# Optimization experiments

Hardware: AMD Instinct MI355X
Metric: run time of the kernel (lower is better)

Reference implementation:

```python
import jax, jax.numpy as jnp
import numpy as np

TAU = 0.8
LAMBDA_BALANCE = 0.05
EPS = 1e-8


def setup_inputs() -> dict:
    key = jax.random.key(0)
    ks = jax.random.split(key, 8)
    B, Din, Dh, Dout, E = 8192, 1024, 2048, 1024, 8
    x = jax.random.normal(ks[0], (B, Din), jnp.float32)
    # gumbel noise for F.gumbel_softmax: g = -log(-log(U)), U~Uniform(0,1)
    u = jax.random.uniform(ks[1], (B, E), jnp.float32, 1e-6, 1.0 - 1e-6)
    gumbel = -jnp.log(-jnp.log(u))
    gate_w = jax.random.normal(ks[2], (Din, E), jnp.float32) * 0.02
    gate_b = jnp.zeros((E,), jnp.float32)
    w1 = jax.random.normal(ks[3], (E, Din, Dh), jnp.float32) * (1.0 / np.sqrt(Din))
    b1 = jnp.zeros((E, Dh), jnp.float32)
    w2 = jax.random.normal(ks[4], (E, Dh, Dout), jnp.float32) * (1.0 / np.sqrt(Dh))
    b2 = jnp.zeros((E, Dout), jnp.float32)
    return dict(x=x, gumbel=gumbel, gate_w=gate_w, gate_b=gate_b,
                w1=w1, b1=b1, w2=w2, b2=b2)


def reference(x, gumbel, gate_w, gate_b, w1, b1, w2, b2):
    # gating logits [B, E]
    logits = x @ gate_w + gate_b
    # gumbel-softmax (soft), tau=0.8 -> selection probs (selection_policy='soft')
    probs = jax.nn.softmax((logits + gumbel) / TAU, axis=1)
    # load-balancing auxiliary loss
    router_probs = jax.nn.softmax(logits / TAU, axis=1)
    importance = router_probs.mean(axis=0)  # [E]
    load = probs.mean(axis=0)               # [E]
    importance_cv = jnp.std(importance, ddof=1) / (importance.mean() + EPS)
    load_cv = jnp.std(load, ddof=1) / (load.mean() + EPS)
    E = probs.shape[1]
    switch_loss = E * jnp.sum(importance * load)
    aux_loss = (switch_loss + importance_cv + load_cv) * LAMBDA_BALANCE
    # dense all-expert MLP stack: h [E,B,Dh], eo [E,B,Dout]
    h = jax.nn.relu(jnp.einsum('bd,edh->ebh', x, w1) + b1[:, None, :])
    eo = jnp.einsum('ebh,eho->ebo', h, w2) + b2[:, None, :]
    # bmm combine: expert_outputs [B, Dout, E] @ probs [B, E, 1] -> [B, Dout]
    output = jnp.einsum('ebo,be->bo', eo, probs)
    return output, aux_loss
```

## Files before the change

### kernel.cpp

```cpp
#include <hip/hip_runtime.h>

typedef __attribute__((ext_vector_type(4))) float f4;
typedef __attribute__((ext_vector_type(8))) short s8;

__device__ inline float b2f(unsigned int u) {
    unsigned int v = u << 16;
    float f;
    __builtin_memcpy(&f, &v, 4);
    return f;
}
__device__ inline unsigned short f2b(float f) {
    unsigned int u;
    __builtin_memcpy(&u, &f, 4);
    unsigned int r = u + 0x7fffu + ((u >> 16) & 1u);
    return (unsigned short)(r >> 16);
}
__device__ inline void async16(const void* g, void* l) {
    __builtin_amdgcn_global_load_lds(
        (const __attribute__((address_space(1))) unsigned int*)g,
        (__attribute__((address_space(3))) unsigned int*)l, 16, 0, 0);
}

#define B_ROWS 8192
#define DIN 1024
#define DH 2048
#define DOUT 1024
#define NE 8
#define NCAT 16384

#define MFMA16(a, b, c) __builtin_amdgcn_mfma_f32_16x16x32_bf16(a, b, c, 0, 0, 0)

__global__ __launch_bounds__(64) void detect_dtype(const unsigned short* __restrict__ p, int* __restrict__ flag)
{
    const int lane = threadIdx.x;
    int sane = 0;
    for (int i = lane; i < 4096; i += 64) {
        const float a = fabsf(b2f(p[i]));
        if (a > 1e-30f && a < 1e3f) sane++;
    }
    for (int off = 32; off; off >>= 1) sane += __shfl_xor(sane, off, 64);
    if (lane == 0) *flag = (sane < 3600) ? 1 : 0;
}

__global__ __launch_bounds__(256) void normalize_kernel(const void* __restrict__ src,
                                                        unsigned short* __restrict__ dst,
                                                        const int* __restrict__ flag, int n)
{
    const int i = blockIdx.x * 256 + threadIdx.x;
    if (i >= n) return;
    if (*flag) dst[i] = f2b(((const float*)src)[i]);
    else       dst[i] = ((const unsigned short*)src)[i];
}

__global__ __launch_bounds__(256) void gating_kernel(
    const unsigned short* __restrict__ x, const unsigned short* __restrict__ gum,
    const unsigned short* __restrict__ gw, const unsigned short* __restrict__ gb,
    float* __restrict__ probs, float* __restrict__ partials)
{
    const int t = threadIdx.x, wave = t >> 6, lane = t & 63;
    float sp = 0.f, sr = 0.f;
    const int base = blockIdx.x * 32 + wave * 8;
    for (int rr = 0; rr < 8; rr++) {
        const int b = base + rr;
        float acc[8];
#pragma unroll
        for (int e = 0; e < 8; e++) acc[e] = 0.f;
        for (int kk = 0; kk < 16; kk++) {
            const int k = kk * 64 + lane;
            const float xv = b2f(x[(size_t)b * DIN + k]);
            const uint4 wv = *(const uint4*)(gw + (size_t)k * 8);
            acc[0] += xv * b2f(wv.x & 0xffffu); acc[1] += xv * b2f(wv.x >> 16);
            acc[2] += xv * b2f(wv.y & 0xffffu); acc[3] += xv * b2f(wv.y >> 16);
            acc[4] += xv * b2f(wv.z & 0xffffu); acc[5] += xv * b2f(wv.z >> 16);
            acc[6] += xv * b2f(wv.w & 0xffffu); acc[7] += xv * b2f(wv.w >> 16);
        }
#pragma unroll
        for (int e = 0; e < 8; e++)
            for (int off = 32; off; off >>= 1) acc[e] += __shfl_xor(acc[e], off, 64);
        float lg[8], p1[8], p2[8];
        float m1 = -1e30f, m2 = -1e30f;
#pragma unroll
        for (int e = 0; e < 8; e++) {
            lg[e] = acc[e] + b2f(gb[e]);
            p1[e] = (lg[e] + b2f(gum[(size_t)b * 8 + e])) * 1.25f;
            p2[e] = lg[e] * 1.25f;
            m1 = fmaxf(m1, p1[e]); m2 = fmaxf(m2, p2[e]);
        }
        float s1 = 0.f, s2 = 0.f;
#pragma unroll
        for (int e = 0; e < 8; e++) {
            p1[e] = expf(p1[e] - m1); s1 += p1[e];
            p2[e] = expf(p2[e] - m2); s2 += p2[e];
        }
        const float i1 = 1.f / s1, i2 = 1.f / s2;
        if (lane < 8) {
            const float pv = p1[lane] * i1;
            probs[(size_t)b * 8 + lane] = pv;
            sp += pv;
            sr += p2[lane] * i2;
        }
    }
    __shared__ float red[4][16];
    if (lane < 8) { red[wave][lane] = sp; red[wave][8 + lane] = sr; }
    __syncthreads();
    if (t < 16)
        partials[blockIdx.x * 16 + t] = red[0][t] + red[1][t] + red[2][t] + red[3][t];
}

__global__ void aux_finalize(const float* __restrict__ partials, void* __restrict__ outp,
                             const int* __restrict__ flag)
{
    __shared__ float fin[16];
    const int t = threadIdx.x;
    if (t < 16) {
        float s = 0.f;
        for (int i = 0; i < 256; i++) s += partials[i * 16 + t];
        fin[t] = s;
    }
    __syncthreads();
    if (t == 0) {
        float ld[8], im[8];
        for (int e = 0; e < 8; e++) { ld[e] = fin[e] / 8192.f; im[e] = fin[8 + e] / 8192.f; }
        float mi = 0.f, ml = 0.f;
        for (int e = 0; e < 8; e++) { mi += im[e]; ml += ld[e]; }
        mi *= 0.125f; ml *= 0.125f;
        float vi = 0.f, vl = 0.f, sw = 0.f;
        for (int e = 0; e < 8; e++) {
            vi += (im[e] - mi) * (im[e] - mi);
            vl += (ld[e] - ml) * (ld[e] - ml);
            sw += im[e] * ld[e];
        }
        const float cvi = sqrtf(vi / 7.f) / (mi + 1e-8f);
        const float cvl = sqrtf(vl / 7.f) / (ml + 1e-8f);
        const float aux = (8.f * sw + cvi + cvl) * 0.05f;
        if (*flag) ((float*)outp)[8388608] = aux;
        else       ((unsigned short*)outp)[8388608] = f2b(aux);
    }
}

__global__ __launch_bounds__(256) void transpose_cvt(
    const void* __restrict__ src, unsigned short* __restrict__ out,
    int R, int C, int ldOut, size_t outEStride, const int* __restrict__ flag)
{
    __shared__ unsigned short tile[64][65];
    const int e = blockIdx.z;
    const size_t eoff = (size_t)e * R * C;
    unsigned short* op = out + (size_t)e * outEStride;
    const int fl = *flag;
    const int tx = threadIdx.x, ty = threadIdx.y;
    const int r0 = blockIdx.y * 64, c0 = blockIdx.x * 64;
    if (fl) {
        const float* in = (const float*)src + eoff;
#pragma unroll
        for (int i = 0; i < 16; i++) {
            const int r = ty + i * 4;
            tile[r][tx] = f2b(in[(size_t)(r0 + r) * C + c0 + tx]);
        }
    } else {
        const unsigned short* in = (const unsigned short*)src + eoff;
#pragma unroll
        for (int i = 0; i < 16; i++) {
            const int r = ty + i * 4;
            tile[r][tx] = in[(size_t)(r0 + r) * C + c0 + tx];
        }
    }
    __syncthreads();
#pragma unroll
    for (int i = 0; i < 16; i++) {
        const int c = ty + i * 4;
        op[(size_t)(c0 + c) * ldOut + r0 + tx] = tile[tx][c];
    }
}


__global__ __launch_bounds__(256) void gemm_h(
    const unsigned short* __restrict__ A,
    const unsigned short* __restrict__ Bt,
    const unsigned short* __restrict__ bias,
    const float* __restrict__ probs,
    unsigned short* __restrict__ outH)
{
    constexpr int K = DIN;
    __shared__ __align__(16) char smem[32768];

    const int t = threadIdx.x;
    int bid = blockIdx.y * gridDim.x + blockIdx.x;
    const int cpx = (gridDim.x * gridDim.y) >> 3;
    bid = (bid & 7) * cpx + (bid >> 3);
    const int bx = bid % gridDim.x, by = bid / gridDim.x;
    const int m0 = bx * 128, n0 = by * 128;

    const int wave = t >> 6, lane = t & 63;
    const int wm = wave >> 1, wn = wave & 1;
    const int quad = lane >> 4, l16 = lane & 15;

    f4 acc[4][4];
#pragma unroll
    for (int i = 0; i < 4; i++)
#pragma unroll
        for (int j = 0; j < 4; j++) { acc[i][j][0] = 0.f; acc[i][j][1] = 0.f; acc[i][j][2] = 0.f; acc[i][j][3] = 0.f; }

    const int rA = t >> 2;
    const int cb = (((t & 3) ^ ((t >> 3) & 3)) * 16);
    const char* pA0 = (const char*)(A + (size_t)(m0 + rA) * K) + cb;
    const char* pA1 = pA0 + (size_t)64 * K * 2;
    const char* pB0 = (const char*)(Bt + (size_t)(n0 + rA) * K) + cb;
    const char* pB1 = pB0 + (size_t)64 * K * 2;

    const int skey = ((quad ^ ((l16 >> 1) & 3)) << 4);
    int aoff[4], boff[4];
#pragma unroll
    for (int i = 0; i < 4; i++) {
        aoff[i] = (wm * 64 + i * 16 + l16) * 64 + skey;
        boff[i] = (wn * 64 + i * 16 + l16) * 64 + skey;
    }

    {
        char* s = smem;
        async16(pA0, s + t * 16);
        async16(pA1, s + 4096 + t * 16);
        async16(pB0, s + 8192 + t * 16);
        async16(pB1, s + 12288 + t * 16);
    }
    __syncthreads();

    int cur = 0;
    for (int k0 = 0; k0 < K; k0 += 32) {
        if (k0 + 32 < K) {
            char* s = smem + (cur ^ 1) * 16384;
            const size_t kb = (size_t)(k0 + 32) * 2;
            async16(pA0 + kb, s + t * 16);
            async16(pA1 + kb, s + 4096 + t * 16);
            async16(pB0 + kb, s + 8192 + t * 16);
            async16(pB1 + kb, s + 12288 + t * 16);
        }
        const char* s = smem + cur * 16384;
        s8 av[4], bv[4];
#pragma unroll
        for (int i = 0; i < 4; i++) av[i] = *(const s8*)(s + aoff[i]);
#pragma unroll
        for (int j = 0; j < 4; j++) bv[j] = *(const s8*)(s + 8192 + boff[j]);
#pragma unroll
        for (int i = 0; i < 4; i++)
#pragma unroll
            for (int j = 0; j < 4; j++)
                acc[i][j] = MFMA16(av[i], bv[j], acc[i][j]);
        __syncthreads();
        cur ^= 1;
    }

#pragma unroll
    for (int i = 0; i < 4; i++) {
        const int gmB = m0 + wm * 64 + i * 16 + quad * 4;
#pragma unroll
        for (int j = 0; j < 4; j++) {
            const int gn = n0 + wn * 64 + j * 16 + l16;
            const int e = gn >> 11;
            const float bval = b2f(bias[gn]);
#pragma unroll
            for (int r = 0; r < 4; r++) {
                const int gm = gmB + r;
                const float pb = probs[(size_t)gm * 8 + e];
                float v = acc[i][j][r] + bval;
                v = fmaxf(v, 0.f) * pb;
                outH[(size_t)gm * NCAT + gn] = f2b(v);
            }
        }
    }
}

__global__ __launch_bounds__(512, 4) void gemm_o3(
    const unsigned short* __restrict__ A,
    const unsigned short* __restrict__ Bt,
    float* __restrict__ partial, int rows, int klen)
{
    constexpr int K = NCAT;
    __shared__ __align__(16) char smem[49152];
    const int t = threadIdx.x;
    const int w = t >> 6, l = t & 63;
    const int l15 = l & 15, q = l >> 4;
    const int wm = w >> 2, wn = w & 3;

    const int m0 = blockIdx.x * 128, n0 = blockIdx.y * 256;
    const int kstart = blockIdx.z * klen;

    const int srow = l >> 2;
    const int gr = ((l & 3) ^ ((l >> 3) & 3)) * 8;
    const unsigned short* pa  = A  + (size_t)(m0 + w * 16 + srow) * K + kstart + gr;
    const unsigned short* pb0 = Bt + (size_t)(n0 + w * 32 + srow) * K + kstart + gr;
    const unsigned short* pb1 = pb0 + (size_t)16 * K;

    const int skey = ((q ^ ((l15 >> 1) & 3)) << 4);
    int aoff[4], boff[4];
#pragma unroll
    for (int mf = 0; mf < 4; mf++) aoff[mf] = (wm * 64 + mf * 16 + l15) * 64 + skey;
#pragma unroll
    for (int nf = 0; nf < 4; nf++) boff[nf] = (wn * 64 + nf * 16 + l15) * 64 + skey;

    f4 acc[4][4];
#pragma unroll
    for (int i = 0; i < 4; i++)
#pragma unroll
        for (int j = 0; j < 4; j++) { acc[i][j][0] = 0.f; acc[i][j][1] = 0.f; acc[i][j][2] = 0.f; acc[i][j][3] = 0.f; }

    {
        char* Ab = smem; char* Bb = smem + 8192;
        async16(pa,  Ab + w * 1024 + (l & 63) * 16);
        async16(pb0, Bb + w * 2048 + (l & 63) * 16);
        async16(pb1, Bb + w * 2048 + 1024 + (l & 63) * 16);
    }
    __syncthreads();

    int cur = 0;
    for (int k0 = 0; k0 < klen; k0 += 32) {
        if (k0 + 32 < klen) {
            char* Ab = smem + (cur ^ 1) * 24576; char* Bb = Ab + 8192;
            const int kn = k0 + 32;
            async16(pa + kn,  Ab + w * 1024 + (l & 63) * 16);
            async16(pb0 + kn, Bb + w * 2048 + (l & 63) * 16);
            async16(pb1 + kn, Bb + w * 2048 + 1024 + (l & 63) * 16);
        }
        const char* Ab = smem + cur * 24576;
        const char* Bb = Ab + 8192;
        s8 Af[4], Bf[4];
#pragma unroll
        for (int mf = 0; mf < 4; mf++) Af[mf] = *(const s8*)(Ab + aoff[mf]);
#pragma unroll
        for (int nf = 0; nf < 4; nf++) Bf[nf] = *(const s8*)(Bb + boff[nf]);
#pragma unroll
        for (int mf = 0; mf < 4; mf++)
#pragma unroll
            for (int nf = 0; nf < 4; nf++)
                acc[mf][nf] = MFMA16(Af[mf], Bf[nf], acc[mf][nf]);
        __syncthreads();
        cur ^= 1;
    }

    float* pp = partial + (size_t)blockIdx.z * rows * DOUT;
#pragma unroll
    for (int mf = 0; mf < 4; mf++) {
        const int gmB = m0 + wm * 64 + mf * 16 + q * 4;
#pragma unroll
        for (int nf = 0; nf < 4; nf++) {
            const int gn = n0 + wn * 64 + nf * 16 + l15;
#pragma unroll
            for (int r = 0; r < 4; r++)
                pp[(size_t)(gmB + r) * DOUT + gn] = acc[mf][nf][r];
        }
    }
}

__global__ __launch_bounds__(256) void out_finalize(
    const float* __restrict__ partial, const unsigned short* __restrict__ b2,
    const float* __restrict__ probs, void* __restrict__ outp, size_t outOff,
    const int* __restrict__ flag, int rows, int nks)
{
    const int idx = blockIdx.x * 256 + threadIdx.x;
    if (idx >= rows * DOUT) return;
    const int m = idx >> 10, n = idx & (DOUT - 1);
    float v = 0.f;
    for (int ks = 0; ks < nks; ks++)
        v += partial[(size_t)ks * rows * DOUT + idx];
    const f4 p0 = *(const f4*)(probs + (size_t)m * 8);
    const f4 p1 = *(const f4*)(probs + (size_t)m * 8 + 4);
    v += p0[0] * b2f(b2[n])            + p0[1] * b2f(b2[DOUT + n])
       + p0[2] * b2f(b2[2 * DOUT + n]) + p0[3] * b2f(b2[3 * DOUT + n])
       + p1[0] * b2f(b2[4 * DOUT + n]) + p1[1] * b2f(b2[5 * DOUT + n])
       + p1[2] * b2f(b2[6 * DOUT + n]) + p1[3] * b2f(b2[7 * DOUT + n]);
    const size_t oi = outOff + ((size_t)m * DOUT) + n;
    if (*flag) ((float*)outp)[oi] = v;
    else       ((unsigned short*)outp)[oi] = f2b(v);
}

extern "C" void kernel_launch(void* const* d_in, const int* in_sizes, int n_in,
                              void* d_out, int out_size, void* d_ws, size_t ws_size,
                              hipStream_t stream)
{
    const void* x   = d_in[0];
    const void* gum = d_in[1];
    const void* gw  = d_in[2];
    const void* gb  = d_in[3];
    const void* w1  = d_in[4];
    const void* b1  = d_in[5];
    const void* w2  = d_in[6];
    const void* b2  = d_in[7];

    char* ws = (char*)d_ws;
    size_t cur = 0;
    auto alloc = [&](size_t bytes) { size_t p = cur; cur = (cur + bytes + 255) & ~(size_t)255; return p; };

    int* flag              = (int*)(ws + alloc(256));
    float* probs           = (float*)(ws + alloc(8192 * 8 * 4));
    float* partials        = (float*)(ws + alloc(256 * 16 * 4));
    unsigned short* xn     = (unsigned short*)(ws + alloc((size_t)B_ROWS * DIN * 2));
    unsigned short* gumn   = (unsigned short*)(ws + alloc((size_t)B_ROWS * 8 * 2));
    unsigned short* gwn    = (unsigned short*)(ws + alloc((size_t)DIN * 8 * 2));
    unsigned short* gbn    = (unsigned short*)(ws + alloc(8 * 2));
    unsigned short* b1n    = (unsigned short*)(ws + alloc((size_t)NE * DH * 2));
    unsigned short* b2n    = (unsigned short*)(ws + alloc((size_t)NE * DOUT * 2));
    unsigned short* w1Tcat = (unsigned short*)(ws + alloc((size_t)NCAT * DIN * 2));
    unsigned short* w2Tcat = (unsigned short*)(ws + alloc((size_t)DOUT * NCAT * 2));
    const size_t fixed = cur;

    int R = B_ROWS, KS;
    for (;;) {
        KS = 16384 / R;
        const size_t need = fixed + (size_t)R * (NCAT * 2) + (size_t)KS * R * DOUT * 4;
        if (R <= 512 || need <= ws_size) break;
        R >>= 1;
    }
    const int klen = 16384 / KS;
    unsigned short* Hcat = (unsigned short*)(ws + fixed);
    float* partial = (float*)(ws + fixed + (size_t)R * (NCAT * 2));

    detect_dtype<<<1, 64, 0, stream>>>((const unsigned short*)x, flag);

    normalize_kernel<<<(B_ROWS * DIN + 255) / 256, 256, 0, stream>>>(x, xn, flag, B_ROWS * DIN);
    normalize_kernel<<<(B_ROWS * 8 + 255) / 256, 256, 0, stream>>>(gum, gumn, flag, B_ROWS * 8);
    normalize_kernel<<<(DIN * 8 + 255) / 256, 256, 0, stream>>>(gw, gwn, flag, DIN * 8);
    normalize_kernel<<<1, 256, 0, stream>>>(gb, gbn, flag, 8);
    normalize_kernel<<<(NE * DH + 255) / 256, 256, 0, stream>>>(b1, b1n, flag, NE * DH);
    normalize_kernel<<<(NE * DOUT + 255) / 256, 256, 0, stream>>>(b2, b2n, flag, NE * DOUT);

    gating_kernel<<<256, 256, 0, stream>>>(xn, gumn, gwn, gbn, probs, partials);
    aux_finalize<<<1, 64, 0, stream>>>(partials, d_out, flag);

    transpose_cvt<<<dim3(DH / 64, DIN / 64, NE), dim3(64, 4), 0, stream>>>(
        w1, w1Tcat, DIN, DH, DIN, (size_t)DH * DIN, flag);
    transpose_cvt<<<dim3(DOUT / 64, DH / 64, NE), dim3(64, 4), 0, stream>>>(
        w2, w2Tcat, DH, DOUT, NCAT, (size_t)DH, flag);

    for (int c0 = 0; c0 < B_ROWS; c0 += R) {
        gemm_h<<<dim3(R / 128, NCAT / 128), 256, 0, stream>>>(
            xn + (size_t)c0 * DIN, w1Tcat, b1n, probs + (size_t)c0 * 8, Hcat);
        gemm_o3<<<dim3(R / 128, DOUT / 256, KS), 512, 0, stream>>>(
            Hcat, w2Tcat, partial, R, klen);
        out_finalize<<<(R * DOUT) / 256, 256, 0, stream>>>(
            partial, b2n, probs + (size_t)c0 * 8, d_out, (size_t)c0 * DOUT, flag, R, KS);
    }
}
```

Baseline: 1.020 ms.

## Process experts in pairs with per-expert GEMMs accumulating output in place

Replaces the concatenated-expert H GEMM and the split-K second GEMM with its partial-reduction pass. The new flow processes two experts at a time, computes H for each, then runs a per-expert 128x128 GEMM that adds into an fp32 output accumulator; the last expert writes the final output. This removes the split-K partial buffers and the separate finalize kernel. In exchange there are more launches, the fp32 accumulator is read and written once per expert, and the second GEMM grid is smaller per launch (512 blocks).

```diff
diff --git a/kernel.cpp b/kernel.cpp
--- a/kernel.cpp
+++ b/kernel.cpp
@@ -172,24 +172,39 @@
     }
 }
 
-
-__global__ __launch_bounds__(256) void gemm_h(
+template<int K, int LDB, int EPI>
+__global__ __launch_bounds__(256) void gemm128(
     const unsigned short* __restrict__ A,
-    const unsigned short* __restrict__ Bt,
-    const unsigned short* __restrict__ bias,
+    const unsigned short* __restrict__ BtBase,
+    const unsigned short* __restrict__ biasBase,
     const float* __restrict__ probs,
-    unsigned short* __restrict__ outH)
-{
-    constexpr int K = DIN;
+    int eBase,
+    unsigned short* __restrict__ outH0,
+    float* __restrict__ outacc,
+    int first,
+    void* __restrict__ outp,
+    const int* __restrict__ flag)
+{
     __shared__ __align__(16) char smem[32768];
+    __shared__ float probsS[128];
 
     const int t = threadIdx.x;
+    const int ez = (EPI == 0) ? blockIdx.z : 0;
+    const int e = eBase + ez;
+
     int bid = blockIdx.y * gridDim.x + blockIdx.x;
     const int cpx = (gridDim.x * gridDim.y) >> 3;
     bid = (bid & 7) * cpx + (bid >> 3);
     const int bx = bid % gridDim.x, by = bid / gridDim.x;
     const int m0 = bx * 128, n0 = by * 128;
 
+    const unsigned short* Bt;
+    const unsigned short* bias;
+    if (EPI == 0) { Bt = BtBase + (size_t)e * DH * DIN; bias = biasBase + e * DH; }
+    else          { Bt = BtBase + (size_t)e * DH;       bias = biasBase + e * DOUT; }
+
+    if (t < 128) probsS[t] = probs[(size_t)(m0 + t) * 8 + e];
+
     const int wave = t >> 6, lane = t & 63;
     const int wm = wave >> 1, wn = wave & 1;
     const int quad = lane >> 4, l16 = lane & 15;
@@ -204,8 +219,8 @@
     const int cb = (((t & 3) ^ ((t >> 3) & 3)) * 16);
     const char* pA0 = (const char*)(A + (size_t)(m0 + rA) * K) + cb;
     const char* pA1 = pA0 + (size_t)64 * K * 2;
-    const char* pB0 = (const char*)(Bt + (size_t)(n0 + rA) * K) + cb;
-    const char* pB1 = pB0 + (size_t)64 * K * 2;
+    const char* pB0 = (const char*)(Bt + (size_t)(n0 + rA) * LDB) + cb;
+    const char* pB1 = pB0 + (size_t)64 * LDB * 2;
 
     const int skey = ((quad ^ ((l16 >> 1) & 3)) << 4);
     int aoff[4], boff[4];
@@ -249,127 +264,48 @@
         cur ^= 1;
     }
 
-#pragma unroll
-    for (int i = 0; i < 4; i++) {
-        const int gmB = m0 + wm * 64 + i * 16 + quad * 4;
+    if (EPI == 0) {
+        unsigned short* outH = outH0 + (size_t)ez * B_ROWS * DH;
 #pragma unroll
         for (int j = 0; j < 4; j++) {
             const int gn = n0 + wn * 64 + j * 16 + l16;
-            const int e = gn >> 11;
             const float bval = b2f(bias[gn]);
 #pragma unroll
-            for (int r = 0; r < 4; r++) {
-                const int gm = gmB + r;
-                const float pb = probs[(size_t)gm * 8 + e];
-                float v = acc[i][j][r] + bval;
-                v = fmaxf(v, 0.f) * pb;
-                outH[(size_t)gm * NCAT + gn] = f2b(v);
+            for (int i = 0; i < 4; i++) {
+                const int lmB = wm * 64 + i * 16 + quad * 4;
+#pragma unroll
+                for (int r = 0; r < 4; r++) {
+                    const int lm = lmB + r;
+                    const float v = fmaxf(acc[i][j][r] + bval, 0.f) * probsS[lm];
+                    outH[(size_t)(m0 + lm) * DH + gn] = f2b(v);
+                }
             }
         }
-    }
-}
-
-__global__ __launch_bounds__(512, 4) void gemm_o3(
-    const unsigned short* __restrict__ A,
-    const unsigned short* __restrict__ Bt,
-    float* __restrict__ partial, int rows, int klen)
-{
-    constexpr int K = NCAT;
-    __shared__ __align__(16) char smem[49152];
-    const int t = threadIdx.x;
-    const int w = t >> 6, l = t & 63;
-    const int l15 = l & 15, q = l >> 4;
-    const int wm = w >> 2, wn = w & 3;
-
-    const int m0 = blockIdx.x * 128, n0 = blockIdx.y * 256;
-    const int kstart = blockIdx.z * klen;
-
-    const int srow = l >> 2;
-    const int gr = ((l & 3) ^ ((l >> 3) & 3)) * 8;
-    const unsigned short* pa  = A  + (size_t)(m0 + w * 16 + srow) * K + kstart + gr;
-    const unsigned short* pb0 = Bt + (size_t)(n0 + w * 32 + srow) * K + kstart + gr;
-    const unsigned short* pb1 = pb0 + (size_t)16 * K;
-
-    const int skey = ((q ^ ((l15 >> 1) & 3)) << 4);
-    int aoff[4], boff[4];
-#pragma unroll
-    for (int mf = 0; mf < 4; mf++) aoff[mf] = (wm * 64 + mf * 16 + l15) * 64 + skey;
-#pragma unroll
-    for (int nf = 0; nf < 4; nf++) boff[nf] = (wn * 64 + nf * 16 + l15) * 64 + skey;
-
-    f4 acc[4][4];
-#pragma unroll
-    for (int i = 0; i < 4; i++)
-#pragma unroll
-        for (int j = 0; j < 4; j++) { acc[i][j][0] = 0.f; acc[i][j][1] = 0.f; acc[i][j][2] = 0.f; acc[i][j][3] = 0.f; }
-
-    {
-        char* Ab = smem; char* Bb = smem + 8192;
-        async16(pa,  Ab + w * 1024 + (l & 63) * 16);
-        async16(pb0, Bb + w * 2048 + (l & 63) * 16);
-        async16(pb1, Bb + w * 2048 + 1024 + (l & 63) * 16);
-    }
-    __syncthreads();
-
-    int cur = 0;
-    for (int k0 = 0; k0 < klen; k0 += 32) {
-        if (k0 + 32 < klen) {
-            char* Ab = smem + (cur ^ 1) * 24576; char* Bb = Ab + 8192;
-            const int kn = k0 + 32;
-            async16(pa + kn,  Ab + w * 1024 + (l & 63) * 16);
-            async16(pb0 + kn, Bb + w * 2048 + (l & 63) * 16);
-            async16(pb1 + kn, Bb + w * 2048 + 1024 + (l & 63) * 16);
-        }
-        const char* Ab = smem + cur * 24576;
-        const char* Bb = Ab + 8192;
-        s8 Af[4], Bf[4];
-#pragma unroll
-        for (int mf = 0; mf < 4; mf++) Af[mf] = *(const s8*)(Ab + aoff[mf]);
-#pragma unroll
-        for (int nf = 0; nf < 4; nf++) Bf[nf] = *(const s8*)(Bb + boff[nf]);
-#pragma unroll
-        for (int mf = 0; mf < 4; mf++)
-#pragma unroll
-            for (int nf = 0; nf < 4; nf++)
-                acc[mf][nf] = MFMA16(Af[mf], Bf[nf], acc[mf][nf]);
-        __syncthreads();
-        cur ^= 1;
-    }
-
-    float* pp = partial + (size_t)blockIdx.z * rows * DOUT;
-#pragma unroll
-    for (int mf = 0; mf < 4; mf++) {
-        const int gmB = m0 + wm * 64 + mf * 16 + q * 4;
-#pragma unroll
-        for (int nf = 0; nf < 4; nf++) {
-            const int gn = n0 + wn * 64 + nf * 16 + l15;
-#pragma unroll
-            for (int r = 0; r < 4; r++)
-                pp[(size_t)(gmB + r) * DOUT + gn] = acc[mf][nf][r];
-        }
-    }
-}
-
-__global__ __launch_bounds__(256) void out_finalize(
-    const float* __restrict__ partial, const unsigned short* __restrict__ b2,
-    const float* __restrict__ probs, void* __restrict__ outp, size_t outOff,
-    const int* __restrict__ flag, int rows, int nks)
-{
-    const int idx = blockIdx.x * 256 + threadIdx.x;
-    if (idx >= rows * DOUT) return;
-    const int m = idx >> 10, n = idx & (DOUT - 1);
-    float v = 0.f;
-    for (int ks = 0; ks < nks; ks++)
-        v += partial[(size_t)ks * rows * DOUT + idx];
-    const f4 p0 = *(const f4*)(probs + (size_t)m * 8);
-    const f4 p1 = *(const f4*)(probs + (size_t)m * 8 + 4);
-    v += p0[0] * b2f(b2[n])            + p0[1] * b2f(b2[DOUT + n])
-       + p0[2] * b2f(b2[2 * DOUT + n]) + p0[3] * b2f(b2[3 * DOUT + n])
-       + p1[0] * b2f(b2[4 * DOUT + n]) + p1[1] * b2f(b2[5 * DOUT + n])
-       + p1[2] * b2f(b2[6 * DOUT + n]) + p1[3] * b2f(b2[7 * DOUT + n]);
-    const size_t oi = outOff + ((size_t)m * DOUT) + n;
-    if (*flag) ((float*)outp)[oi] = v;
-    else       ((unsigned short*)outp)[oi] = f2b(v);
+    } else {
+        const int fl = (EPI == 2) ? *flag : 0;
+#pragma unroll
+        for (int j = 0; j < 4; j++) {
+            const int gn = n0 + wn * 64 + j * 16 + l16;
+            const float b2v = b2f(bias[gn]);
+#pragma unroll
+            for (int i = 0; i < 4; i++) {
+                const int lmB = wm * 64 + i * 16 + quad * 4;
+#pragma unroll
+                for (int r = 0; r < 4; r++) {
+                    const int lm = lmB + r;
+                    const size_t idx = (size_t)(m0 + lm) * DOUT + gn;
+                    float v = acc[i][j][r] + probsS[lm] * b2v;
+                    if (!first) v += outacc[idx];
+                    if (EPI == 1) {
+                        outacc[idx] = v;
+                    } else {
+                        if (fl) ((float*)outp)[idx] = v;
+                        else    ((unsigned short*)outp)[idx] = f2b(v);
+                    }
+                }
+            }
+        }
+    }
 }
 
 extern "C" void kernel_launch(void* const* d_in, const int* in_sizes, int n_in,
@@ -400,18 +336,9 @@
     unsigned short* b2n    = (unsigned short*)(ws + alloc((size_t)NE * DOUT * 2));
     unsigned short* w1Tcat = (unsigned short*)(ws + alloc((size_t)NCAT * DIN * 2));
     unsigned short* w2Tcat = (unsigned short*)(ws + alloc((size_t)DOUT * NCAT * 2));
-    const size_t fixed = cur;
-
-    int R = B_ROWS, KS;
-    for (;;) {
-        KS = 16384 / R;
-        const size_t need = fixed + (size_t)R * (NCAT * 2) + (size_t)KS * R * DOUT * 4;
-        if (R <= 512 || need <= ws_size) break;
-        R >>= 1;
-    }
-    const int klen = 16384 / KS;
-    unsigned short* Hcat = (unsigned short*)(ws + fixed);
-    float* partial = (float*)(ws + fixed + (size_t)R * (NCAT * 2));
+    unsigned short* Hpair  = (unsigned short*)(ws + alloc((size_t)2 * B_ROWS * DH * 2));
+    float* outacc          = (float*)(ws + alloc((size_t)B_ROWS * DOUT * 4));
+    (void)cur;
 
     detect_dtype<<<1, 64, 0, stream>>>((const unsigned short*)x, flag);
 
@@ -430,12 +357,19 @@
     transpose_cvt<<<dim3(DOUT / 64, DH / 64, NE), dim3(64, 4), 0, stream>>>(
         w2, w2Tcat, DH, DOUT, NCAT, (size_t)DH, flag);
 
-    for (int c0 = 0; c0 < B_ROWS; c0 += R) {
-        gemm_h<<<dim3(R / 128, NCAT / 128), 256, 0, stream>>>(
-            xn + (size_t)c0 * DIN, w1Tcat, b1n, probs + (size_t)c0 * 8, Hcat);
-        gemm_o3<<<dim3(R / 128, DOUT / 256, KS), 512, 0, stream>>>(
-            Hcat, w2Tcat, partial, R, klen);
-        out_finalize<<<(R * DOUT) / 256, 256, 0, stream>>>(
-            partial, b2n, probs + (size_t)c0 * 8, d_out, (size_t)c0 * DOUT, flag, R, KS);
-    }
-}
+    for (int p = 0; p < 4; p++) {
+        const int e0 = 2 * p;
+        gemm128<DIN, DIN, 0><<<dim3(B_ROWS / 128, DH / 128, 2), 256, 0, stream>>>(
+            xn, w1Tcat, b1n, probs, e0, Hpair, nullptr, 0, nullptr, nullptr);
+        for (int z = 0; z < 2; z++) {
+            const int e = e0 + z;
+            const unsigned short* He = Hpair + (size_t)z * B_ROWS * DH;
+            if (e < NE - 1)
+                gemm128<DH, NCAT, 1><<<dim3(B_ROWS / 128, DOUT / 128), 256, 0, stream>>>(
+                    He, w2Tcat, b2n, probs, e, nullptr, outacc, e == 0, nullptr, nullptr);
+            else
+                gemm128<DH, NCAT, 2><<<dim3(B_ROWS / 128, DOUT / 128), 256, 0, stream>>>(
+                    He, w2Tcat, b2n, probs, e, nullptr, outacc, 0, d_out, flag);
+        }
+    }
+}
```

Measured after the change: 1.193 ms. 17.0% more time.
